# Performance work log

Hardware: AMD Instinct MI355X
Metric: run time of the kernel (lower is better)

Reference implementation:

```python
import jax, jax.numpy as jnp
import numpy as np

V, D, H, L, S, B = 50257, 512, 8, 6, 1024, 2
DH = D // H
SCALE = float(np.sqrt(D))  # module scales by sqrt(embed_dim), not sqrt(head_dim)


def _ln(x, g, b):
    m = jnp.mean(x, -1, keepdims=True)
    v = jnp.mean((x - m) ** 2, -1, keepdims=True)
    return (x - m) * jax.lax.rsqrt(v + 1e-5) * g + b


def setup_inputs():
    key = jax.random.key(0)
    ks = jax.random.split(key, 12)
    s = 0.02
    idx_sequences = jax.random.randint(ks[0], (B, S + 1), 0, V)
    masks = jnp.ones((B, S), jnp.int32)
    tok_emb = (jax.random.normal(ks[1], (V, D), jnp.float32) * s).at[0].set(0.0)  # pad_idx=0 row zeroed
    pos_emb = jax.random.normal(ks[2], (1, S, D), jnp.float32) * s
    Wq = jax.random.normal(ks[3], (L, D, D), jnp.float32) * s
    Wk = jax.random.normal(ks[4], (L, D, D), jnp.float32) * s
    Wv = jax.random.normal(ks[5], (L, D, D), jnp.float32) * s
    Wo = jax.random.normal(ks[6], (L, D, D), jnp.float32) * s
    bq = jnp.zeros((L, D)); bk = jnp.zeros((L, D)); bv = jnp.zeros((L, D)); bo = jnp.zeros((L, D))
    ln1_g = jnp.ones((L, D)); ln1_b = jnp.zeros((L, D))
    W1 = jax.random.normal(ks[7], (L, D, 4 * D), jnp.float32) * s
    b1 = jnp.zeros((L, 4 * D))
    W2 = jax.random.normal(ks[8], (L, 4 * D, D), jnp.float32) * s
    b2 = jnp.zeros((L, D))
    ln2_g = jnp.ones((L, D)); ln2_b = jnp.zeros((L, D))
    lnf_g = jnp.ones((D,)); lnf_b = jnp.zeros((D,))
    head_w = jax.random.normal(ks[9], (D, V), jnp.float32) * s
    return dict(idx_sequences=idx_sequences, masks=masks, tok_emb=tok_emb, pos_emb=pos_emb,
                Wq=Wq, bq=bq, Wk=Wk, bk=bk, Wv=Wv, bv=bv, Wo=Wo, bo=bo,
                ln1_g=ln1_g, ln1_b=ln1_b, W1=W1, b1=b1, W2=W2, b2=b2,
                ln2_g=ln2_g, ln2_b=ln2_b, lnf_g=lnf_g, lnf_b=lnf_b, head_w=head_w)


def reference(idx_sequences, masks, tok_emb, pos_emb, Wq, bq, Wk, bk, Wv, bv, Wo, bo,
              ln1_g, ln1_b, W1, b1, W2, b2, ln2_g, ln2_b, lnf_g, lnf_b, head_w):
    inputs = idx_sequences[:, :-1]   # (B,S)
    targets = idx_sequences[:, 1:]   # (B,S)
    m = masks.astype(tok_emb.dtype)  # (B,S) 1=valid
    x = (tok_emb[inputs] + pos_emb) * m[..., None]  # zero padded positions (dropout p=0)
    causal = jnp.tril(jnp.ones((S, S), bool))

    def block(x, p):
        wq, bq_, wk, bk_, wv, bv_, wo, bo_, g1, be1, w1, b1_, w2, b2_, g2, be2 = p
        h = _ln(x, g1, be1)
        q = (h @ wq + bq_).reshape(B, S, H, DH).transpose(0, 2, 1, 3)  # (B,H,S,DH)
        k = (h @ wk + bk_).reshape(B, S, H, DH).transpose(0, 2, 1, 3)
        v = (h @ wv + bv_).reshape(B, S, H, DH).transpose(0, 2, 1, 3)
        sc = jnp.einsum('bhqd,bhkd->bhqk', q, k) / SCALE
        sc = jnp.where(causal, sc, -jnp.inf)
        a = jax.nn.softmax(sc, axis=-1)
        o = jnp.einsum('bhqk,bhkd->bhqd', a, v).transpose(0, 2, 1, 3).reshape(B, S, D)
        x = x + o @ wo + bo_
        h2 = _ln(x, g2, be2)
        x = x + (jax.nn.gelu(h2 @ w1 + b1_, approximate=False) @ w2 + b2_)
        return x, None

    x, _ = jax.lax.scan(block, x, (Wq, bq, Wk, bk, Wv, bv, Wo, bo,
                                   ln1_g, ln1_b, W1, b1, W2, b2, ln2_g, ln2_b))
    logits = _ln(x, lnf_g, lnf_b) @ head_w  # (B,S,V)
    logp = jax.nn.log_softmax(logits, axis=-1)
    nll = -jnp.take_along_axis(logp, targets[..., None], axis=-1)[..., 0]  # (B,S)
    loss = jnp.mean(nll * m)  # masked_fill(mask==0, 0).mean()
    return logits, loss
```

## Files before the change

### kernel.cpp

```cpp
#include <hip/hip_runtime.h>
#include <hip/hip_bf16.h>
#include <math.h>

constexpr int Vv   = 50257;
constexpr int Vpad = 50304;
constexpr int Dd   = 512;
constexpr int Hh   = 8;
constexpr int Ll   = 6;
constexpr int Ss   = 1024;
constexpr int Bb   = 2;
constexpr int NT   = Bb * Ss;
constexpr int Dff  = 2048;
constexpr float INV_SCALE = 0.04419417382415922f;

typedef __hip_bfloat16 bf16;
typedef __attribute__((ext_vector_type(8))) short bf16x8;
typedef __attribute__((ext_vector_type(4))) float f32x4;

__device__ inline float wave_sum(float x) {
#pragma unroll
  for (int off = 32; off > 0; off >>= 1) x += __shfl_xor(x, off, 64);
  return x;
}

__device__ inline void gl_lds16(const bf16* g, bf16* l) {
  __builtin_amdgcn_global_load_lds((__attribute__((address_space(1))) void*)g,
                                   (__attribute__((address_space(3))) void*)l,
                                   16, 0, 0);
}

__global__ __launch_bounds__(256) void transpose_bf16(
    const float* __restrict__ src, bf16* __restrict__ dst,
    int K, int N, int Npad, long srcStride, long dstStride, float scale) {
  __shared__ float tile[32][33];
  const float* s = src + (size_t)blockIdx.z * srcStride;
  bf16* d = dst + (size_t)blockIdx.z * dstStride;
  int n0 = blockIdx.x * 32, k0 = blockIdx.y * 32;
  int tr = threadIdx.x >> 5, tc = threadIdx.x & 31;
#pragma unroll
  for (int i = 0; i < 4; i++) {
    int k = k0 + tr + i * 8, n = n0 + tc;
    tile[tr + i * 8][tc] = (k < K && n < N) ? s[(size_t)k * N + n] * scale : 0.f;
  }
  __syncthreads();
#pragma unroll
  for (int i = 0; i < 4; i++) {
    int n = n0 + tr + i * 8, k = k0 + tc;
    if (n < Npad && k < K) d[(size_t)n * K + k] = __float2bfloat16(tile[tc][tr + i * 8]);
  }
}

__global__ void concat_bias(const float* __restrict__ bq, const float* __restrict__ bk,
                            const float* __restrict__ bv, float* __restrict__ dst) {
  int i = blockIdx.x * 256 + threadIdx.x;
  if (i >= Ll * 1536) return;
  int l = i / 1536, j = i - l * 1536;
  float v = (j < 512) ? bq[l * 512 + j] * INV_SCALE
          : (j < 1024) ? bk[l * 512 + j - 512]
                       : bv[l * 512 + j - 1024];
  dst[i] = v;
}

__global__ void embed_kernel(const int* __restrict__ idx, const int* __restrict__ masks,
                             const float* __restrict__ tok, const float* __restrict__ pos,
                             float* __restrict__ x) {
  int i = blockIdx.x * blockDim.x + threadIdx.x;
  if (i >= NT * Dd) return;
  int d = i & (Dd - 1);
  int row = i >> 9;
  int s = row & (Ss - 1);
  int b = row >> 10;
  int t = idx[b * (Ss + 1) + s];
  float m = (float)masks[row];
  x[i] = (tok[(size_t)t * Dd + d] + pos[s * Dd + d]) * m;
}

__global__ __launch_bounds__(256) void ln_kernel(const float* __restrict__ x,
                                                 const float* __restrict__ g,
                                                 const float* __restrict__ b,
                                                 bf16* __restrict__ out) {
  int row = blockIdx.x * 4 + (threadIdx.x >> 6);
  int lane = threadIdx.x & 63;
  const float* xr = x + (size_t)row * Dd;
  float vals[8];
  float s = 0.f;
#pragma unroll
  for (int i = 0; i < 8; i++) { vals[i] = xr[lane + i * 64]; s += vals[i]; }
  s = wave_sum(s);
  float mean = s * (1.f / Dd);
  float vs = 0.f;
#pragma unroll
  for (int i = 0; i < 8; i++) { float dd = vals[i] - mean; vs += dd * dd; }
  vs = wave_sum(vs);
  float rstd = rsqrtf(vs * (1.f / Dd) + 1e-5f);
  bf16* orow = out + (size_t)row * Dd;
#pragma unroll
  for (int i = 0; i < 8; i++) {
    int d = lane + i * 64;
    orow[d] = __float2bfloat16((vals[i] - mean) * rstd * g[d] + b[d]);
  }
}

__global__ __launch_bounds__(256) void mfma_gemm(
    const bf16* __restrict__ A, const bf16* __restrict__ Bt,
    const float* __restrict__ bias, const float* __restrict__ resid,
    float* __restrict__ Cf, bf16* __restrict__ Cb,
    int M, int N, int K, int act) {
  __shared__ bf16 As[128 * 32];
  __shared__ bf16 Bs[128 * 32];
  const int t = threadIdx.x;
  const int w = t >> 6, lane = t & 63;
  const int m0 = blockIdx.y * 128, n0 = blockIdx.x * 128;
  const int rr = lane >> 2;
  const int cc = (lane & 3) * 8;
  const bf16* ap0 = A  + (size_t)(m0 + w * 32 + rr) * K + cc;
  const bf16* ap1 = ap0 + (size_t)16 * K;
  const bf16* bp0 = Bt + (size_t)(n0 + w * 32 + rr) * K + cc;
  const bf16* bp1 = bp0 + (size_t)16 * K;
  bf16* as0 = As + w * 32 * 32;
  bf16* as1 = as0 + 16 * 32;
  bf16* bs0 = Bs + w * 32 * 32;
  bf16* bs1 = bs0 + 16 * 32;
  const int wr = (w >> 1) * 64, wc = (w & 1) * 64;
  const int lm = lane & 15, lk = (lane >> 4) * 8;
  f32x4 acc[4][4];
#pragma unroll
  for (int i = 0; i < 4; i++)
#pragma unroll
    for (int j = 0; j < 4; j++) acc[i][j] = (f32x4){0.f, 0.f, 0.f, 0.f};

  for (int k0 = 0; k0 < K; k0 += 32) {
    __syncthreads();
    gl_lds16(ap0 + k0, as0);
    gl_lds16(ap1 + k0, as1);
    gl_lds16(bp0 + k0, bs0);
    gl_lds16(bp1 + k0, bs1);
    __syncthreads();
    bf16x8 af[4], bg[4];
#pragma unroll
    for (int i = 0; i < 4; i++)
      af[i] = *(const bf16x8*)(As + (wr + i * 16 + lm) * 32 + lk);
#pragma unroll
    for (int j = 0; j < 4; j++)
      bg[j] = *(const bf16x8*)(Bs + (wc + j * 16 + lm) * 32 + lk);
#pragma unroll
    for (int i = 0; i < 4; i++)
#pragma unroll
      for (int j = 0; j < 4; j++)
        acc[i][j] = __builtin_amdgcn_mfma_f32_16x16x32_bf16(af[i], bg[j], acc[i][j], 0, 0, 0);
  }

  const int r4 = (lane >> 4) * 4;
#pragma unroll
  for (int i = 0; i < 4; i++) {
#pragma unroll
    for (int j = 0; j < 4; j++) {
      int col = n0 + wc + j * 16 + lm;
      if (col >= N) continue;
      float bi = bias ? bias[col] : 0.f;
#pragma unroll
      for (int r = 0; r < 4; r++) {
        int row = m0 + wr + i * 16 + r4 + r;
        float v = acc[i][j][r] + bi;
        if (act) v = 0.5f * v * (1.f + erff(v * 0.70710678118654752f));
        if (resid) v += resid[(size_t)row * N + col];
        if (Cf) Cf[(size_t)row * N + col] = v;
        else    Cb[(size_t)row * N + col] = __float2bfloat16(v);
      }
    }
  }
}

__global__ __launch_bounds__(256) void v_transpose(const bf16* __restrict__ qkv,
                                                   bf16* __restrict__ vT) {
  __shared__ alignas(16) bf16 tile[64][72];
  const int bx = blockIdx.x, bh = blockIdx.y;
  const int b = bh >> 3, h = bh & 7;
  const int t = threadIdx.x;
  {
    int sl = t >> 2, dg = (t & 3) * 16;
    const bf16* src = qkv + (size_t)(b * Ss + bx * 64 + sl) * 1536 + 1024 + h * 64 + dg;
    *(bf16x8*)&tile[sl][dg]     = *(const bf16x8*)(src);
    *(bf16x8*)&tile[sl][dg + 8] = *(const bf16x8*)(src + 8);
  }
  __syncthreads();
  {
    int dl = t >> 2, sg = (t & 3) * 16;
    bf16* dst = vT + ((size_t)bh * 64 + dl) * Ss + bx * 64 + sg;
    alignas(16) bf16 tmp[16];
#pragma unroll
    for (int i = 0; i < 16; i++) tmp[i] = tile[sg + i][dl];
    *(bf16x8*)dst       = *(bf16x8*)tmp;
    *(bf16x8*)(dst + 8) = *(bf16x8*)(tmp + 8);
  }
}

__global__ __launch_bounds__(128) void attn_mfma(const bf16* __restrict__ qkv,
                                                 const bf16* __restrict__ vT,
                                                 bf16* __restrict__ o) {
  __shared__ alignas(16) bf16 P[2][16][72];
  const int t = threadIdx.x;
  const int w = t >> 6, lane = t & 63;
  const int hi = lane >> 4, lm = lane & 15;
  const int qt = 31 - (int)blockIdx.x;
  const int bh = blockIdx.y;
  const int b = bh >> 3, h = bh & 7;
  const int hcol = h * 64;
  const size_t rb = (size_t)b * Ss * 1536;
  const int q0 = qt * 32 + w * 16;

  bf16x8 qf[2];
  {
    const bf16* qp = qkv + rb + (size_t)(q0 + lm) * 1536 + hcol + hi * 8;
    qf[0] = *(const bf16x8*)qp;
    qf[1] = *(const bf16x8*)(qp + 32);
  }
  f32x4 Oacc[4];
#pragma unroll
  for (int i = 0; i < 4; i++) Oacc[i] = (f32x4){0.f, 0.f, 0.f, 0.f};
  float m[4] = {-INFINITY, -INFINITY, -INFINITY, -INFINITY};
  float l[4] = {0.f, 0.f, 0.f, 0.f};

  const int ct = qt >> 1;
  const bf16* kbase = qkv + rb + 512 + hcol;
  const bf16* vbase = vT + (size_t)bh * 64 * Ss;

  for (int c = 0; c <= ct; c++) {
    f32x4 S[4];
#pragma unroll
    for (int tt = 0; tt < 4; tt++) S[tt] = (f32x4){0.f, 0.f, 0.f, 0.f};
#pragma unroll
    for (int tt = 0; tt < 4; tt++) {
      const bf16* kp = kbase + (size_t)(c * 64 + tt * 16 + lm) * 1536 + hi * 8;
      bf16x8 k0 = *(const bf16x8*)kp;
      bf16x8 k1 = *(const bf16x8*)(kp + 32);
      S[tt] = __builtin_amdgcn_mfma_f32_16x16x32_bf16(qf[0], k0, S[tt], 0, 0, 0);
      S[tt] = __builtin_amdgcn_mfma_f32_16x16x32_bf16(qf[1], k1, S[tt], 0, 0, 0);
    }
    if (c == ct) {
#pragma unroll
      for (int tt = 0; tt < 4; tt++) {
        int key = c * 64 + tt * 16 + lm;
#pragma unroll
        for (int r = 0; r < 4; r++) {
          if (key > q0 + hi * 4 + r) S[tt][r] = -INFINITY;
        }
      }
    }
    float mn[4], al[4];
#pragma unroll
    for (int r = 0; r < 4; r++) {
      float mx = fmaxf(fmaxf(S[0][r], S[1][r]), fmaxf(S[2][r], S[3][r]));
#pragma unroll
      for (int off = 1; off < 16; off <<= 1) mx = fmaxf(mx, __shfl_xor(mx, off, 64));
      mn[r] = fmaxf(m[r], mx);
      al[r] = __expf(m[r] - mn[r]);
      m[r] = mn[r];
    }
    float p[4][4];
#pragma unroll
    for (int tt = 0; tt < 4; tt++)
#pragma unroll
      for (int r = 0; r < 4; r++) p[tt][r] = __expf(S[tt][r] - mn[r]);
#pragma unroll
    for (int r = 0; r < 4; r++) {
      float s = p[0][r] + p[1][r] + p[2][r] + p[3][r];
#pragma unroll
      for (int off = 1; off < 16; off <<= 1) s += __shfl_xor(s, off, 64);
      l[r] = l[r] * al[r] + s;
    }
#pragma unroll
    for (int i = 0; i < 4; i++) {
      Oacc[i][0] *= al[0]; Oacc[i][1] *= al[1];
      Oacc[i][2] *= al[2]; Oacc[i][3] *= al[3];
    }
#pragma unroll
    for (int tt = 0; tt < 4; tt++)
#pragma unroll
      for (int r = 0; r < 4; r++)
        P[w][hi * 4 + r][tt * 16 + lm] = __float2bfloat16(p[tt][r]);
#pragma unroll
    for (int e = 0; e < 2; e++) {
      bf16x8 pa = *(const bf16x8*)&P[w][lm][e * 32 + hi * 8];
#pragma unroll
      for (int tt = 0; tt < 4; tt++) {
        const bf16* vp = vbase + (size_t)(tt * 16 + lm) * Ss + c * 64 + e * 32 + hi * 8;
        bf16x8 vf = *(const bf16x8*)vp;
        Oacc[tt] = __builtin_amdgcn_mfma_f32_16x16x32_bf16(pa, vf, Oacc[tt], 0, 0, 0);
      }
    }
  }
  float inv[4] = {1.f / l[0], 1.f / l[1], 1.f / l[2], 1.f / l[3]};
  bf16* ob = o + (size_t)(b * Ss + q0) * Dd + hcol;
#pragma unroll
  for (int tt = 0; tt < 4; tt++)
#pragma unroll
    for (int r = 0; r < 4; r++)
      ob[(size_t)(hi * 4 + r) * Dd + tt * 16 + lm] = __float2bfloat16(Oacc[tt][r] * inv[r]);
}

__global__ __launch_bounds__(256) void nll_kernel(const float* __restrict__ logits,
                                                  const int* __restrict__ idx,
                                                  const int* __restrict__ masks,
                                                  float* __restrict__ row_nll) {
  __shared__ float red[256];
  int row = blockIdx.x;
  int b = row >> 10, s = row & (Ss - 1);
  const float* lr = logits + (size_t)row * Vv;
  float mx = -INFINITY;
  for (int j = threadIdx.x; j < Vv; j += 256) mx = fmaxf(mx, lr[j]);
  red[threadIdx.x] = mx;
  __syncthreads();
  for (int st = 128; st > 0; st >>= 1) {
    if (threadIdx.x < st) red[threadIdx.x] = fmaxf(red[threadIdx.x], red[threadIdx.x + st]);
    __syncthreads();
  }
  mx = red[0];
  __syncthreads();
  float sum = 0.f;
  for (int j = threadIdx.x; j < Vv; j += 256) sum += __expf(lr[j] - mx);
  red[threadIdx.x] = sum;
  __syncthreads();
  for (int st = 128; st > 0; st >>= 1) {
    if (threadIdx.x < st) red[threadIdx.x] += red[threadIdx.x + st];
    __syncthreads();
  }
  if (threadIdx.x == 0) {
    int target = idx[b * (Ss + 1) + s + 1];
    float nll = logf(red[0]) + mx - lr[target];
    row_nll[row] = nll * (float)masks[row];
  }
}

__global__ __launch_bounds__(256) void loss_reduce_kernel(const float* __restrict__ row_nll,
                                                          float* __restrict__ out_loss) {
  __shared__ float red[256];
  float s = 0.f;
  for (int i = threadIdx.x; i < NT; i += 256) s += row_nll[i];
  red[threadIdx.x] = s;
  __syncthreads();
  for (int st = 128; st > 0; st >>= 1) {
    if (threadIdx.x < st) red[threadIdx.x] += red[threadIdx.x + st];
    __syncthreads();
  }
  if (threadIdx.x == 0) out_loss[0] = red[0] * (1.f / NT);
}

extern "C" void kernel_launch(void* const* d_in, const int* in_sizes, int n_in,
                              void* d_out, int out_size, void* d_ws, size_t ws_size,
                              hipStream_t stream) {
  const int*   idx   = (const int*)d_in[0];
  const int*   masks = (const int*)d_in[1];
  const float* tok   = (const float*)d_in[2];
  const float* pos   = (const float*)d_in[3];
  const float* Wq    = (const float*)d_in[4];
  const float* bq    = (const float*)d_in[5];
  const float* Wk    = (const float*)d_in[6];
  const float* bk    = (const float*)d_in[7];
  const float* Wv    = (const float*)d_in[8];
  const float* bv    = (const float*)d_in[9];
  const float* Wo    = (const float*)d_in[10];
  const float* bo    = (const float*)d_in[11];
  const float* ln1g  = (const float*)d_in[12];
  const float* ln1b  = (const float*)d_in[13];
  const float* W1    = (const float*)d_in[14];
  const float* b1    = (const float*)d_in[15];
  const float* W2    = (const float*)d_in[16];
  const float* b2    = (const float*)d_in[17];
  const float* ln2g  = (const float*)d_in[18];
  const float* ln2b  = (const float*)d_in[19];
  const float* lnfg  = (const float*)d_in[20];
  const float* lnfb  = (const float*)d_in[21];
  const float* headw = (const float*)d_in[22];

  float* out = (float*)d_out;

  char* p = (char*)d_ws;
  auto alloc = [&](size_t bytes) { char* r = p; p += (bytes + 255) & ~255ull; return r; };
  float* x     = (float*)alloc((size_t)NT * Dd * 4);
  bf16*  h     = (bf16*) alloc((size_t)NT * Dd * 2);
  bf16*  qkvb  = (bf16*) alloc((size_t)NT * 1536 * 2);
  bf16*  vT    = (bf16*) alloc((size_t)Bb * Hh * 64 * Ss * 2);
  bf16*  ob    = (bf16*) alloc((size_t)NT * Dd * 2);
  bf16*  mlp   = (bf16*) alloc((size_t)NT * Dff * 2);
  float* rnll  = (float*)alloc((size_t)NT * 4);
  bf16*  WqkvT = (bf16*) alloc((size_t)Ll * 1536 * 512 * 2);
  bf16*  WoT   = (bf16*) alloc((size_t)Ll * 512 * 512 * 2);
  bf16*  W1T   = (bf16*) alloc((size_t)Ll * 2048 * 512 * 2);
  bf16*  W2T   = (bf16*) alloc((size_t)Ll * 512 * 2048 * 2);
  bf16*  headT = (bf16*) alloc((size_t)Vpad * 512 * 2);
  float* bqkvc = (float*)alloc((size_t)Ll * 1536 * 4);

  const long DD = (long)Dd * Dd;
  transpose_bf16<<<dim3(16, 16, Ll), 256, 0, stream>>>(Wq, WqkvT,               512, 512, 512,  DD, 1536L * 512, INV_SCALE);
  transpose_bf16<<<dim3(16, 16, Ll), 256, 0, stream>>>(Wk, WqkvT + 512 * 512,   512, 512, 512,  DD, 1536L * 512, 1.f);
  transpose_bf16<<<dim3(16, 16, Ll), 256, 0, stream>>>(Wv, WqkvT + 1024 * 512,  512, 512, 512,  DD, 1536L * 512, 1.f);
  transpose_bf16<<<dim3(16, 16, Ll), 256, 0, stream>>>(Wo, WoT,                 512, 512, 512,  DD, DD, 1.f);
  transpose_bf16<<<dim3(64, 16, Ll), 256, 0, stream>>>(W1, W1T,                 512, 2048, 2048, (long)512 * 2048, (long)2048 * 512, 1.f);
  transpose_bf16<<<dim3(16, 64, Ll), 256, 0, stream>>>(W2, W2T,                 2048, 512, 512, (long)2048 * 512, (long)512 * 2048, 1.f);
  transpose_bf16<<<dim3(Vpad / 32, 16, 1), 256, 0, stream>>>(headw, headT,      512, Vv, Vpad,  0, 0, 1.f);
  concat_bias<<<(Ll * 1536 + 255) / 256, 256, 0, stream>>>(bq, bk, bv, bqkvc);

  embed_kernel<<<(NT * Dd + 255) / 256, 256, 0, stream>>>(idx, masks, tok, pos, x);

  for (int l = 0; l < Ll; l++) {
    ln_kernel<<<NT / 4, 256, 0, stream>>>(x, ln1g + (size_t)l * Dd, ln1b + (size_t)l * Dd, h);
    mfma_gemm<<<dim3(12, 16), 256, 0, stream>>>(h, WqkvT + (size_t)l * 1536 * 512,
        bqkvc + (size_t)l * 1536, nullptr, nullptr, qkvb, NT, 1536, 512, 0);
    v_transpose<<<dim3(Ss / 64, Bb * Hh), 256, 0, stream>>>(qkvb, vT);
    attn_mfma<<<dim3(32, Bb * Hh), 128, 0, stream>>>(qkvb, vT, ob);
    mfma_gemm<<<dim3(4, 16), 256, 0, stream>>>(ob, WoT + (size_t)l * DD,
        bo + (size_t)l * Dd, x, x, nullptr, NT, 512, 512, 0);
    ln_kernel<<<NT / 4, 256, 0, stream>>>(x, ln2g + (size_t)l * Dd, ln2b + (size_t)l * Dd, h);
    mfma_gemm<<<dim3(16, 16), 256, 0, stream>>>(h, W1T + (size_t)l * Dff * Dd,
        b1 + (size_t)l * Dff, nullptr, nullptr, mlp, NT, 2048, 512, 1);
    mfma_gemm<<<dim3(4, 16), 256, 0, stream>>>(mlp, W2T + (size_t)l * Dff * Dd,
        b2 + (size_t)l * Dd, x, x, nullptr, NT, 512, 2048, 0);
  }

  ln_kernel<<<NT / 4, 256, 0, stream>>>(x, lnfg, lnfb, h);
  mfma_gemm<<<dim3(Vpad / 128, 16), 256, 0, stream>>>(h, headT, nullptr, nullptr,
      out, nullptr, NT, Vv, 512, 0);

  nll_kernel<<<NT, 256, 0, stream>>>(out, idx, masks, rnll);
  loss_reduce_kernel<<<1, 256, 0, stream>>>(rnll, out + (size_t)NT * Vv);
}
```

Baseline: 2.235 ms.

## Fuse V transpose and softmax partials into GEMM epilogues, split-K with atomics

The GEMM gains a swizzled 1D block mapping for L2 locality. Its QKV epilogue now writes the transposed V directly, which removes the v_transpose kernel. The Wo and W2 projections use split-K with atomicAdd into the residual stream, giving more blocks for the small-N GEMMs. The head GEMM epilogue emits per-64-column max/sum-exp partials, so the NLL kernel reduces about 786 partials per row instead of rereading the full logits row twice. The costs are strided uncoalesced vT stores, atomic contention, nondeterministic accumulation order, and a partials buffer aliased onto qkvb.

Measured after the change: 1.823 ms. -18.4%, faster.

```diff
diff --git a/kernel.cpp b/kernel.cpp
--- a/kernel.cpp
+++ b/kernel.cpp
@@ -11,6 +11,7 @@
 constexpr int Bb   = 2;
 constexpr int NT   = Bb * Ss;
 constexpr int Dff  = 2048;
+constexpr int PCH  = Vpad / 64;
 constexpr float INV_SCALE = 0.04419417382415922f;
 
 typedef __hip_bfloat16 bf16;
@@ -105,12 +106,18 @@
     const bf16* __restrict__ A, const bf16* __restrict__ Bt,
     const float* __restrict__ bias, const float* __restrict__ resid,
     float* __restrict__ Cf, bf16* __restrict__ Cb,
-    int M, int N, int K, int act) {
+    bf16* __restrict__ vTout, float* __restrict__ partials,
+    float* __restrict__ Catomic,
+    int N, int K, int act, int klen) {
   __shared__ bf16 As[128 * 32];
   __shared__ bf16 Bs[128 * 32];
   const int t = threadIdx.x;
   const int w = t >> 6, lane = t & 63;
-  const int m0 = blockIdx.y * 128, n0 = blockIdx.x * 128;
+  const int q8 = gridDim.x >> 3;
+  const int lin = blockIdx.x;
+  const int swz = (lin & 7) * q8 + (lin >> 3);
+  const int m0 = (swz & 15) << 7;
+  const int n0 = (swz >> 4) << 7;
   const int rr = lane >> 2;
   const int cc = (lane & 3) * 8;
   const bf16* ap0 = A  + (size_t)(m0 + w * 32 + rr) * K + cc;
@@ -129,7 +136,9 @@
 #pragma unroll
     for (int j = 0; j < 4; j++) acc[i][j] = (f32x4){0.f, 0.f, 0.f, 0.f};
 
-  for (int k0 = 0; k0 < K; k0 += 32) {
+  const int kbeg = blockIdx.z * klen;
+  const int kend = kbeg + klen;
+  for (int k0 = kbeg; k0 < kend; k0 += 32) {
     __syncthreads();
     gl_lds16(ap0 + k0, as0);
     gl_lds16(ap1 + k0, as1);
@@ -151,6 +160,22 @@
   }
 
   const int r4 = (lane >> 4) * 4;
+  if (Catomic) {
+    const float bs = (blockIdx.z == 0) ? 1.f : 0.f;
+#pragma unroll
+    for (int i = 0; i < 4; i++)
+#pragma unroll
+      for (int j = 0; j < 4; j++) {
+        int col = n0 + wc + j * 16 + lm;
+        float bi = bias[col] * bs;
+#pragma unroll
+        for (int r = 0; r < 4; r++) {
+          int row = m0 + wr + i * 16 + r4 + r;
+          atomicAdd(&Catomic[(size_t)row * N + col], acc[i][j][r] + bi);
+        }
+      }
+    return;
+  }
 #pragma unroll
   for (int i = 0; i < 4; i++) {
 #pragma unroll
@@ -166,32 +191,43 @@
         if (resid) v += resid[(size_t)row * N + col];
         if (Cf) Cf[(size_t)row * N + col] = v;
         else    Cb[(size_t)row * N + col] = __float2bfloat16(v);
+        if (vTout && col >= 1024) {
+          int dcol = col - 1024;
+          int b = row >> 10;
+          vTout[((size_t)((b << 3) + (dcol >> 6)) * 64 + (dcol & 63)) * Ss + (row & (Ss - 1))]
+              = __float2bfloat16(v);
+        }
       }
     }
   }
-}
-
-__global__ __launch_bounds__(256) void v_transpose(const bf16* __restrict__ qkv,
-                                                   bf16* __restrict__ vT) {
-  __shared__ alignas(16) bf16 tile[64][72];
-  const int bx = blockIdx.x, bh = blockIdx.y;
-  const int b = bh >> 3, h = bh & 7;
-  const int t = threadIdx.x;
-  {
-    int sl = t >> 2, dg = (t & 3) * 16;
-    const bf16* src = qkv + (size_t)(b * Ss + bx * 64 + sl) * 1536 + 1024 + h * 64 + dg;
-    *(bf16x8*)&tile[sl][dg]     = *(const bf16x8*)(src);
-    *(bf16x8*)&tile[sl][dg + 8] = *(const bf16x8*)(src + 8);
-  }
-  __syncthreads();
-  {
-    int dl = t >> 2, sg = (t & 3) * 16;
-    bf16* dst = vT + ((size_t)bh * 64 + dl) * Ss + bx * 64 + sg;
-    alignas(16) bf16 tmp[16];
-#pragma unroll
-    for (int i = 0; i < 16; i++) tmp[i] = tile[sg + i][dl];
-    *(bf16x8*)dst       = *(bf16x8*)tmp;
-    *(bf16x8*)(dst + 8) = *(bf16x8*)(tmp + 8);
+  if (partials) {
+#pragma unroll
+    for (int i = 0; i < 4; i++) {
+#pragma unroll
+      for (int r = 0; r < 4; r++) {
+        float mx = -INFINITY;
+#pragma unroll
+        for (int j = 0; j < 4; j++) {
+          int col = n0 + wc + j * 16 + lm;
+          if (col < N) mx = fmaxf(mx, acc[i][j][r]);
+        }
+#pragma unroll
+        for (int off = 1; off < 16; off <<= 1) mx = fmaxf(mx, __shfl_xor(mx, off, 64));
+        float se = 0.f;
+#pragma unroll
+        for (int j = 0; j < 4; j++) {
+          int col = n0 + wc + j * 16 + lm;
+          if (col < N) se += __expf(acc[i][j][r] - mx);
+        }
+#pragma unroll
+        for (int off = 1; off < 16; off <<= 1) se += __shfl_xor(se, off, 64);
+        if (lm == 0) {
+          int row = m0 + wr + i * 16 + r4 + r;
+          int chunk = (n0 + wc) >> 6;
+          ((float2*)partials)[(size_t)row * PCH + chunk] = make_float2(mx, se);
+        }
+      }
+    }
   }
 }
 
@@ -202,8 +238,8 @@
   const int t = threadIdx.x;
   const int w = t >> 6, lane = t & 63;
   const int hi = lane >> 4, lm = lane & 15;
-  const int qt = 31 - (int)blockIdx.x;
-  const int bh = blockIdx.y;
+  const int qt = 31 - (int)blockIdx.y;
+  const int bh = blockIdx.x;
   const int b = bh >> 3, h = bh & 7;
   const int hcol = h * 64;
   const size_t rb = (size_t)b * Ss * 1536;
@@ -299,36 +335,37 @@
       ob[(size_t)(hi * 4 + r) * Dd + tt * 16 + lm] = __float2bfloat16(Oacc[tt][r] * inv[r]);
 }
 
-__global__ __launch_bounds__(256) void nll_kernel(const float* __restrict__ logits,
+__global__ __launch_bounds__(256) void nll_reduce(const float2* __restrict__ partials,
+                                                  const float* __restrict__ logits,
                                                   const int* __restrict__ idx,
                                                   const int* __restrict__ masks,
                                                   float* __restrict__ row_nll) {
-  __shared__ float red[256];
-  int row = blockIdx.x;
-  int b = row >> 10, s = row & (Ss - 1);
-  const float* lr = logits + (size_t)row * Vv;
-  float mx = -INFINITY;
-  for (int j = threadIdx.x; j < Vv; j += 256) mx = fmaxf(mx, lr[j]);
-  red[threadIdx.x] = mx;
+  __shared__ float sm[256], ss[256];
+  const int row = blockIdx.x;
+  const float2* pr = partials + (size_t)row * PCH;
+  float m = -INFINITY, s = 0.f;
+  for (int j = threadIdx.x; j < PCH; j += 256) {
+    float2 p = pr[j];
+    float mn = fmaxf(m, p.x);
+    s = s * __expf(m - mn) + p.y * __expf(p.x - mn);
+    m = mn;
+  }
+  sm[threadIdx.x] = m; ss[threadIdx.x] = s;
   __syncthreads();
   for (int st = 128; st > 0; st >>= 1) {
-    if (threadIdx.x < st) red[threadIdx.x] = fmaxf(red[threadIdx.x], red[threadIdx.x + st]);
+    if (threadIdx.x < st) {
+      float m2 = sm[threadIdx.x + st], s2 = ss[threadIdx.x + st];
+      float mn = fmaxf(sm[threadIdx.x], m2);
+      ss[threadIdx.x] = ss[threadIdx.x] * __expf(sm[threadIdx.x] - mn) + s2 * __expf(m2 - mn);
+      sm[threadIdx.x] = mn;
+    }
     __syncthreads();
   }
-  mx = red[0];
-  __syncthreads();
-  float sum = 0.f;
-  for (int j = threadIdx.x; j < Vv; j += 256) sum += __expf(lr[j] - mx);
-  red[threadIdx.x] = sum;
-  __syncthreads();
-  for (int st = 128; st > 0; st >>= 1) {
-    if (threadIdx.x < st) red[threadIdx.x] += red[threadIdx.x + st];
-    __syncthreads();
-  }
   if (threadIdx.x == 0) {
-    int target = idx[b * (Ss + 1) + s + 1];
-    float nll = logf(red[0]) + mx - lr[target];
-    row_nll[row] = nll * (float)masks[row];
+    int b = row >> 10, sq = row & (Ss - 1);
+    int target = idx[b * (Ss + 1) + sq + 1];
+    float tv = logits[(size_t)row * Vv + target];
+    row_nll[row] = (logf(ss[0]) + sm[0] - tv) * (float)masks[row];
   }
 }
 
@@ -390,6 +427,7 @@
   bf16*  W2T   = (bf16*) alloc((size_t)Ll * 512 * 2048 * 2);
   bf16*  headT = (bf16*) alloc((size_t)Vpad * 512 * 2);
   float* bqkvc = (float*)alloc((size_t)Ll * 1536 * 4);
+  float* parts = (float*)qkvb;
 
   const long DD = (long)Dd * Dd;
   transpose_bf16<<<dim3(16, 16, Ll), 256, 0, stream>>>(Wq, WqkvT,               512, 512, 512,  DD, 1536L * 512, INV_SCALE);
@@ -405,23 +443,26 @@
 
   for (int l = 0; l < Ll; l++) {
     ln_kernel<<<NT / 4, 256, 0, stream>>>(x, ln1g + (size_t)l * Dd, ln1b + (size_t)l * Dd, h);
-    mfma_gemm<<<dim3(12, 16), 256, 0, stream>>>(h, WqkvT + (size_t)l * 1536 * 512,
-        bqkvc + (size_t)l * 1536, nullptr, nullptr, qkvb, NT, 1536, 512, 0);
-    v_transpose<<<dim3(Ss / 64, Bb * Hh), 256, 0, stream>>>(qkvb, vT);
-    attn_mfma<<<dim3(32, Bb * Hh), 128, 0, stream>>>(qkvb, vT, ob);
-    mfma_gemm<<<dim3(4, 16), 256, 0, stream>>>(ob, WoT + (size_t)l * DD,
-        bo + (size_t)l * Dd, x, x, nullptr, NT, 512, 512, 0);
+    mfma_gemm<<<dim3(192, 1, 1), 256, 0, stream>>>(h, WqkvT + (size_t)l * 1536 * 512,
+        bqkvc + (size_t)l * 1536, nullptr, nullptr, qkvb, vT, nullptr, nullptr,
+        1536, 512, 0, 512);
+    attn_mfma<<<dim3(Bb * Hh, 32), 128, 0, stream>>>(qkvb, vT, ob);
+    mfma_gemm<<<dim3(64, 1, 2), 256, 0, stream>>>(ob, WoT + (size_t)l * DD,
+        bo + (size_t)l * Dd, nullptr, nullptr, nullptr, nullptr, nullptr, x,
+        512, 512, 0, 256);
     ln_kernel<<<NT / 4, 256, 0, stream>>>(x, ln2g + (size_t)l * Dd, ln2b + (size_t)l * Dd, h);
-    mfma_gemm<<<dim3(16, 16), 256, 0, stream>>>(h, W1T + (size_t)l * Dff * Dd,
-        b1 + (size_t)l * Dff, nullptr, nullptr, mlp, NT, 2048, 512, 1);
-    mfma_gemm<<<dim3(4, 16), 256, 0, stream>>>(mlp, W2T + (size_t)l * Dff * Dd,
-        b2 + (size_t)l * Dd, x, x, nullptr, NT, 512, 2048, 0);
+    mfma_gemm<<<dim3(256, 1, 1), 256, 0, stream>>>(h, W1T + (size_t)l * Dff * Dd,
+        b1 + (size_t)l * Dff, nullptr, nullptr, mlp, nullptr, nullptr, nullptr,
+        2048, 512, 1, 512);
+    mfma_gemm<<<dim3(64, 1, 4), 256, 0, stream>>>(mlp, W2T + (size_t)l * Dff * Dd,
+        b2 + (size_t)l * Dd, nullptr, nullptr, nullptr, nullptr, nullptr, x,
+        512, 2048, 0, 512);
   }
 
   ln_kernel<<<NT / 4, 256, 0, stream>>>(x, lnfg, lnfb, h);
-  mfma_gemm<<<dim3(Vpad / 128, 16), 256, 0, stream>>>(h, headT, nullptr, nullptr,
-      out, nullptr, NT, Vv, 512, 0);
-
-  nll_kernel<<<NT, 256, 0, stream>>>(out, idx, masks, rnll);
+  mfma_gemm<<<dim3(Vpad / 128 * 16, 1, 1), 256, 0, stream>>>(h, headT, nullptr, nullptr,
+      out, nullptr, nullptr, parts, nullptr, Vv, 512, 0, 512);
+
+  nll_reduce<<<NT, 256, 0, stream>>>((const float2*)parts, out, idx, masks, rnll);
   loss_reduce_kernel<<<1, 256, 0, stream>>>(rnll, out + (size_t)NT * Vv);
 }
```
